# Kernel tuning notes

Hardware: AMD Instinct MI355X
Metric: run time of the kernel (lower is better)

The kernel has to match this reference:

```python
import jax, jax.numpy as jnp
import numpy as np

B, N, C, H, D = 1, 256, 128, 4, 32  # batch, seq, c_z, no_heads, c_hidden
INF = 1e9
LN_EPS = 1e-5


def setup_inputs() -> dict:
    key = jax.random.key(0)
    ks = jax.random.split(key, 8)
    s = 0.02
    return {
        "x": jax.random.normal(ks[0], (B, N, N, C), jnp.float32),
        "mask": jnp.ones((B, N, N), jnp.float32),
        "ln_w": jnp.ones((C,), jnp.float32),
        "ln_b": jnp.zeros((C,), jnp.float32),
        "w_bias": jax.random.normal(ks[1], (H, C), jnp.float32) * s,  # tri-bias linear (no bias)
        "wq": jax.random.normal(ks[2], (C, H, D), jnp.float32) * s,
        "wk": jax.random.normal(ks[3], (C, H, D), jnp.float32) * s,
        "wv": jax.random.normal(ks[4], (C, H, D), jnp.float32) * s,
        "wg": jax.random.normal(ks[5], (C, H, D), jnp.float32) * s,
        "bg": jnp.ones((H * D,), jnp.float32),  # gating bias init = 1 (OpenFold)
        "wo": jax.random.normal(ks[6], (C, H * D), jnp.float32) * s,
        "bo": jnp.zeros((C,), jnp.float32),
    }


def reference(x, mask, ln_w, ln_b, w_bias, wq, wk, wv, wg, bg, wo, bo):
    scale = 1.0 / np.sqrt(D)
    # Ending-node: transpose the two N dims, then operate like starting node
    x_t = jnp.swapaxes(x, 1, 2)          # [B, J, I, C] -> treat as [B, N, N, C]
    m_t = jnp.swapaxes(mask, 1, 2)       # [B, N, N]
    # layer norm over channels
    mu = jnp.mean(x_t, axis=-1, keepdims=True)
    var = jnp.var(x_t, axis=-1, keepdims=True)
    xn = (x_t - mu) * jax.lax.rsqrt(var + LN_EPS) * ln_w + ln_b
    # mask bias: inf * (mask - 1), broadcast over heads and query dim
    mask_bias = INF * (m_t[:, :, None, None, :] - 1.0)     # [B, N, 1, 1, N]
    # triangle bias: linear -> permute_final_dims (2,0,1) -> unsqueeze(-4)
    tri_bias = jnp.einsum("bijc,hc->bhij", xn, w_bias)[:, None]  # [B, 1, H, N, N]
    # gated MHA over the last sequence axis
    q = jnp.einsum("bijc,chd->bijhd", xn, wq) * scale
    k = jnp.einsum("bijc,chd->bijhd", xn, wk)
    v = jnp.einsum("bijc,chd->bijhd", xn, wv)
    a = jnp.einsum("bijhd,bikhd->bihjk", q, k) + mask_bias + tri_bias  # [B,N,H,N,N]
    a = jax.nn.softmax(a, axis=-1)
    o = jnp.einsum("bihjk,bikhd->bijhd", a, v)                        # [B,N,N,H,D]
    g = jax.nn.sigmoid(jnp.einsum("bijc,chd->bijhd", xn, wg) + bg.reshape(H, D))
    o = (o * g).reshape(B, N, N, H * D)
    out = jnp.einsum("bijk,ok->bijo", o, wo) + bo                     # [B,N,N,C]
    return jnp.swapaxes(out, 1, 2)
```

## Files before the change

kernel.cpp:

```cpp
#include <hip/hip_runtime.h>

#define N 256
#define C 128
#define H 4
#define D 32
#define LN_EPS 1e-5f
#define INFB 1e9f
#define SCALE 0.17677669529663687f

typedef __bf16 bf16x8 __attribute__((ext_vector_type(8)));
typedef __bf16 bf16x4 __attribute__((ext_vector_type(4)));
typedef __bf16 bf16x2 __attribute__((ext_vector_type(2)));
typedef _Float16 halfx8 __attribute__((ext_vector_type(8)));
typedef float floatx4 __attribute__((ext_vector_type(4)));

__device__ __forceinline__ floatx4 mfma16(bf16x8 a, bf16x8 b, floatx4 c) {
    return __builtin_amdgcn_mfma_f32_16x16x32_bf16(a, b, c, 0, 0, 0);
}
__device__ __forceinline__ floatx4 mfma16h(halfx8 a, halfx8 b, floatx4 c) {
    return __builtin_amdgcn_mfma_f32_16x16x32_f16(a, b, c, 0, 0, 0);
}

__global__ __launch_bounds__(256) void wt_kernel(
    const float* __restrict__ wq, const float* __restrict__ wk,
    const float* __restrict__ wv, const float* __restrict__ wg,
    const float* __restrict__ wo, __bf16* __restrict__ wTg,
    _Float16* __restrict__ woh)
{
    const int mat = blockIdx.x >> 3, seg = blockIdx.x & 7;
    if (mat == 4) {
        #pragma unroll
        for (int rep = 0; rep < 8; ++rep) {
            const int idx = seg * 2048 + rep * 256 + threadIdx.x;
            woh[idx] = (_Float16)wo[idx];
        }
        return;
    }
    const float* __restrict__ ws_ = (mat == 0) ? wq : (mat == 1) ? wk
                                  : (mat == 2) ? wv : wg;
    #pragma unroll
    for (int rep = 0; rep < 8; ++rep) {
        const int idx = seg * 2048 + rep * 256 + threadIdx.x;
        const int n = idx >> 7, c = idx & 127;
        wTg[mat * 16384 + n * 128 + c] = (__bf16)ws_[c * 128 + n];
    }
}

__global__ __launch_bounds__(256) void ln_kernel(
    const float* __restrict__ x, const float* __restrict__ lnw,
    const float* __restrict__ lnb, const float* __restrict__ wbias,
    __bf16* __restrict__ xn, float* __restrict__ tbp)
{
    const int t = threadIdx.x;
    const int wv = t >> 6, half = (t >> 5) & 1, lane = t & 31;
    const int r = blockIdx.x * 8 + wv * 2 + half;
    const int a = r >> 8, b = r & 255;

    const float4 v = *(const float4*)&x[((size_t)b * N + a) * C + lane * 4];
    float s  = v.x + v.y + v.z + v.w;
    float ss = v.x*v.x + v.y*v.y + v.z*v.z + v.w*v.w;
    #pragma unroll
    for (int o = 16; o; o >>= 1) {
        s  += __shfl_xor(s,  o);
        ss += __shfl_xor(ss, o);
    }
    const float mu  = s * (1.0f / 128.0f);
    const float var = ss * (1.0f / 128.0f) - mu * mu;
    const float rs  = rsqrtf(var + LN_EPS);

    const float4 lw = *(const float4*)&lnw[lane * 4];
    const float4 lb = *(const float4*)&lnb[lane * 4];
    const float y0 = (v.x - mu) * rs * lw.x + lb.x;
    const float y1 = (v.y - mu) * rs * lw.y + lb.y;
    const float y2 = (v.z - mu) * rs * lw.z + lb.z;
    const float y3 = (v.w - mu) * rs * lw.w + lb.w;

    bf16x4 xo;
    xo[0] = (__bf16)y0; xo[1] = (__bf16)y1;
    xo[2] = (__bf16)y2; xo[3] = (__bf16)y3;
    *(bf16x4*)&xn[(size_t)r * C + lane * 4] = xo;

    const int jb   = a >> 4;
    const int lnA  = (b & 15) | (((a & 15) >> 2) << 4);
    const int slot = ((b >> 4) << 2) | (a & 3);
    #pragma unroll
    for (int hh = 0; hh < H; ++hh) {
        const float4 wb4 = *(const float4*)&wbias[hh * C + lane * 4];
        float tv = y0 * wb4.x + y1 * wb4.y + y2 * wb4.z + y3 * wb4.w;
        #pragma unroll
        for (int o = 16; o; o >>= 1) tv += __shfl_xor(tv, o);
        if (lane == 0)
            tbp[(size_t)(((hh * 16 + jb) * 64 + lnA) * 64 + slot)] = tv;
    }
}

__global__ __launch_bounds__(256, 3) void proj_kernel(
    const __bf16* __restrict__ xn, const __bf16* __restrict__ wTg,
    __bf16* __restrict__ qbuf, __bf16* __restrict__ kbuf,
    __bf16* __restrict__ vbuf, __bf16* __restrict__ gbuf)
{
    __shared__ __bf16 Cs[4][64 * 72];

    const int t = threadIdx.x, w = t >> 6, lane = t & 63;
    const int ln16 = lane & 15, quad = lane >> 4;
    const int wr = w >> 1, wc = w & 1;
    const int m_base = blockIdx.x * 128 + wr * 64;
    const int n_base = wc * 64;
    const floatx4 z4 = {0.f, 0.f, 0.f, 0.f};

    const int m = m_base + lane;
    const int i = m >> 8, jk = m & 255;
    __bf16* __restrict__ Cw = &Cs[w][0];

    #pragma unroll 1
    for (int mat = 0; mat < 4; ++mat) {
        const __bf16* __restrict__ wT = wTg + mat * 16384;

        floatx4 Cf[4][4];
        #pragma unroll
        for (int mt = 0; mt < 4; ++mt)
            #pragma unroll
            for (int nt = 0; nt < 4; ++nt) Cf[mt][nt] = z4;

        #pragma unroll
        for (int ks = 0; ks < 4; ++ks) {
            bf16x8 Af[4], Bf[4];
            #pragma unroll
            for (int mt = 0; mt < 4; ++mt)
                Af[mt] = *(const bf16x8*)&xn[(size_t)(m_base + mt*16 + ln16) * 128 + ks*32 + quad*8];
            #pragma unroll
            for (int nt = 0; nt < 4; ++nt)
                Bf[nt] = *(const bf16x8*)&wT[(n_base + nt*16 + ln16) * 128 + ks*32 + quad*8];
            #pragma unroll
            for (int mt = 0; mt < 4; ++mt)
                #pragma unroll
                for (int nt = 0; nt < 4; ++nt)
                    Cf[mt][nt] = mfma16(Af[mt], Bf[nt], Cf[mt][nt]);
        }

        const float scl = (mat == 0) ? SCALE : 1.0f;
        #pragma unroll
        for (int mt = 0; mt < 4; ++mt)
            #pragma unroll
            for (int nt = 0; nt < 4; ++nt)
                #pragma unroll
                for (int r = 0; r < 4; ++r)
                    Cw[(mt*16 + quad*4 + r) * 72 + nt*16 + ln16] =
                        (__bf16)(Cf[mt][nt][r] * scl);

        __bf16* __restrict__ dst = (mat == 0) ? qbuf : (mat == 1) ? kbuf
                                 : (mat == 2) ? vbuf : gbuf;
        #pragma unroll
        for (int hf = 0; hf < 2; ++hf) {
            const int hh = wc * 2 + hf;
            __bf16* __restrict__ drow = dst + (((size_t)i*4 + hh)*256 + jk)*32;
            #pragma unroll
            for (int u = 0; u < 4; ++u)
                *(bf16x8*)&drow[u*8] = *(const bf16x8*)&Cw[lane*72 + hf*32 + u*8];
        }
    }
}

__global__ __launch_bounds__(256, 2) void attn_kernel(
    const float* __restrict__ tbp, const float* __restrict__ mask,
    const float* __restrict__ bg,
    const __bf16* __restrict__ qbuf, const __bf16* __restrict__ kbuf,
    const __bf16* __restrict__ vbuf, const __bf16* __restrict__ gbuf,
    _Float16* __restrict__ ogh)
{
    const int bid = blockIdx.x;
    const int i = bid & 255, h = bid >> 8;
    const int t = threadIdx.x, w = t >> 6, lane = t & 63;
    const int ln16 = lane & 15, quad = lane >> 4;

    __shared__ __align__(16) __bf16 Ks[256 * 32];
    __shared__ __align__(16) __bf16 VT[32 * 264];
    __shared__ __align__(16) __bf16 Pw[4][16 * 40];
    __shared__ float mb[256];

    const size_t hb = (size_t)i * 4 + h;
    const __bf16* __restrict__ qb = qbuf + hb * 8192;
    const __bf16* __restrict__ kb = kbuf + hb * 8192;
    const __bf16* __restrict__ vb = vbuf + hb * 8192;
    const __bf16* __restrict__ gb = gbuf + hb * 8192;

    {
        const int xt = (t & 3) ^ ((t >> 2) & 3);
        #pragma unroll
        for (int u = 0; u < 4; ++u)
            *(bf16x8*)&Ks[t * 32 + ((u ^ xt) * 8)] = *(const bf16x8*)&kb[t * 32 + u * 8];
    }
    #pragma unroll
    for (int u = 0; u < 4; ++u) {
        const bf16x8 vv = *(const bf16x8*)&vb[t * 32 + u * 8];
        #pragma unroll
        for (int e = 0; e < 8; ++e) VT[(u*8 + e) * 264 + t] = vv[e];
    }
    mb[t] = INFB * (mask[(size_t)t * N + i] - 1.0f);
    __syncthreads();

    const float bg0 = bg[h*32 + ln16], bg1 = bg[h*32 + 16 + ln16];

    float mbv[16];
    #pragma unroll
    for (int kt = 0; kt < 16; ++kt) mbv[kt] = mb[kt*16 + ln16];

    const int kq = ((quad ^ ((ln16 & 3) ^ ((ln16 >> 2) & 3))) * 8);

    __bf16* __restrict__ Pww = &Pw[w][0];
    const floatx4 z4 = {0.f, 0.f, 0.f, 0.f};
    _Float16* __restrict__ ogb = ogh + ((size_t)h * 256 + i) * 8192;

    #pragma unroll 1
    for (int jt = 0; jt < 4; ++jt) {
        const int jrow0 = w*64 + jt*16;
        const float* __restrict__ tbl =
            tbp + ((size_t)((h*16 + (w*4 + jt))*64 + lane) << 6);
        const bf16x8 Qf = *(const bf16x8*)&qb[(jrow0 + ln16)*32 + quad*8];

        floatx4 S[16];
        #pragma unroll
        for (int kt = 0; kt < 16; ++kt) {
            const float4 tb4 = *(const float4*)&tbl[kt*4];
            const float mbk = mbv[kt];
            floatx4 c;
            c[0] = mbk + tb4.x;
            c[1] = mbk + tb4.y;
            c[2] = mbk + tb4.z;
            c[3] = mbk + tb4.w;
            const bf16x8 Kf = *(const bf16x8*)&Ks[(kt*16 + ln16)*32 + kq];
            S[kt] = mfma16(Qf, Kf, c);
        }

        float mrow[4], l[4];
        #pragma unroll
        for (int r = 0; r < 4; ++r) {
            float mx = S[0][r];
            #pragma unroll
            for (int kt = 1; kt < 16; ++kt) mx = fmaxf(mx, S[kt][r]);
            #pragma unroll
            for (int off = 1; off < 16; off <<= 1) mx = fmaxf(mx, __shfl_xor(mx, off));
            mrow[r] = mx; l[r] = 0.f;
        }
        #pragma unroll
        for (int kt = 0; kt < 16; ++kt)
            #pragma unroll
            for (int r = 0; r < 4; ++r) {
                const float p = __expf(S[kt][r] - mrow[r]);
                S[kt][r] = p; l[r] += p;
            }
        #pragma unroll
        for (int r = 0; r < 4; ++r)
            #pragma unroll
            for (int off = 1; off < 16; off <<= 1) l[r] += __shfl_xor(l[r], off);

        floatx4 O0 = z4, O1 = z4;
        #pragma unroll
        for (int ch = 0; ch < 8; ++ch) {
            #pragma unroll
            for (int kk = 0; kk < 2; ++kk) {
                const int kt = ch*2 + kk;
                #pragma unroll
                for (int r = 0; r < 4; ++r)
                    Pww[(quad*4 + r)*40 + kk*16 + ln16] = (__bf16)S[kt][r];
            }
            const bf16x8 Af = *(const bf16x8*)&Pww[ln16*40 + quad*8];
            const bf16x8 V0 = *(const bf16x8*)&VT[ln16*264 + ch*32 + quad*8];
            const bf16x8 V1 = *(const bf16x8*)&VT[(16 + ln16)*264 + ch*32 + quad*8];
            O0 = mfma16(Af, V0, O0);
            O1 = mfma16(Af, V1, O1);
        }

        _Float16* Po = (_Float16*)Pww;
        #pragma unroll
        for (int r = 0; r < 4; ++r) {
            const float inv = 1.0f / l[r];
            const int jrow = jrow0 + quad*4 + r;
            const float g0 = (float)gb[jrow*32 + ln16];
            const float g1 = (float)gb[jrow*32 + 16 + ln16];
            const float gate0 = 1.0f / (1.0f + __expf(-(g0 + bg0)));
            const float gate1 = 1.0f / (1.0f + __expf(-(g1 + bg1)));
            Po[(quad*4 + r)*40 + ln16]      = (_Float16)(O0[r] * inv * gate0);
            Po[(quad*4 + r)*40 + 16 + ln16] = (_Float16)(O1[r] * inv * gate1);
        }
        {
            const int rr = lane >> 2, cc = lane & 3;
            const halfx8 ov = *(const halfx8*)&Po[rr*40 + cc*8];
            *(halfx8*)&ogb[(size_t)(jrow0 + rr)*32 + cc*8] = ov;
        }
    }
}

__global__ __launch_bounds__(256, 4) void outproj_kernel(
    const _Float16* __restrict__ og, const _Float16* __restrict__ woh,
    const float* __restrict__ bo, float* __restrict__ out)
{
    const int t = threadIdx.x, w = t >> 6, lane = t & 63;
    const int ln16 = lane & 15, quad = lane >> 4;
    const int wr = w >> 1, wc = w & 1;
    const int m_base = blockIdx.x * 128 + wr * 64;
    const int n_base = wc * 64;

    floatx4 Cf[4][4];
    const floatx4 z4 = {0.f, 0.f, 0.f, 0.f};
    #pragma unroll
    for (int mt = 0; mt < 4; ++mt)
        #pragma unroll
        for (int nt = 0; nt < 4; ++nt) Cf[mt][nt] = z4;

    #pragma unroll
    for (int ks = 0; ks < 4; ++ks) {
        halfx8 Af[4], Bf[4];
        #pragma unroll
        for (int mt = 0; mt < 4; ++mt)
            Af[mt] = *(const halfx8*)&og[(size_t)ks*2097152 + (size_t)(m_base + mt*16 + ln16)*32 + quad*8];
        #pragma unroll
        for (int nt = 0; nt < 4; ++nt)
            Bf[nt] = *(const halfx8*)&woh[(n_base + nt*16 + ln16)*128 + ks*32 + quad*8];
        #pragma unroll
        for (int mt = 0; mt < 4; ++mt)
            #pragma unroll
            for (int nt = 0; nt < 4; ++nt)
                Cf[mt][nt] = mfma16h(Af[mt], Bf[nt], Cf[mt][nt]);
    }

    float bov[4];
    #pragma unroll
    for (int nt = 0; nt < 4; ++nt) bov[nt] = bo[n_base + nt*16 + ln16];

    #pragma unroll
    for (int mt = 0; mt < 4; ++mt)
        #pragma unroll
        for (int r = 0; r < 4; ++r) {
            const int m = m_base + mt*16 + quad*4 + r;
            const size_t orow = (size_t)(m & 255) * 256 + (m >> 8);
            #pragma unroll
            for (int nt = 0; nt < 4; ++nt)
                out[orow*128 + n_base + nt*16 + ln16] = Cf[mt][nt][r] + bov[nt];
        }
}

extern "C" void kernel_launch(void* const* d_in, const int* in_sizes, int n_in,
                              void* d_out, int out_size, void* d_ws, size_t ws_size,
                              hipStream_t stream) {
    const float* x     = (const float*)d_in[0];
    const float* mask  = (const float*)d_in[1];
    const float* lnw   = (const float*)d_in[2];
    const float* lnb   = (const float*)d_in[3];
    const float* wbias = (const float*)d_in[4];
    const float* wq    = (const float*)d_in[5];
    const float* wk    = (const float*)d_in[6];
    const float* wv    = (const float*)d_in[7];
    const float* wg    = (const float*)d_in[8];
    const float* bg    = (const float*)d_in[9];
    const float* wo    = (const float*)d_in[10];
    const float* bo    = (const float*)d_in[11];
    float* out = (float*)d_out;

    char* wsb = (char*)d_ws;
    __bf16*    xn   = (__bf16*)   (wsb);
    float*     tbp  = (float*)    (wsb + 16777216);
    __bf16*    wTg  = (__bf16*)   (wsb + 17825792);
    _Float16*  woh  = (_Float16*) (wsb + 17956864);
    __bf16*    qbuf = (__bf16*)   (wsb + 17989632);
    __bf16*    kbuf = (__bf16*)   (wsb + 34766848);
    __bf16*    vbuf = (__bf16*)   (wsb + 51544064);
    __bf16*    gbuf = (__bf16*)   (wsb + 68321280);
    _Float16*  ogh  = (_Float16*) (wsb + 85098496);

    wt_kernel<<<40, 256, 0, stream>>>(wq, wk, wv, wg, wo, wTg, woh);
    ln_kernel<<<8192, 256, 0, stream>>>(x, lnw, lnb, wbias, xn, tbp);
    proj_kernel<<<512, 256, 0, stream>>>(xn, wTg, qbuf, kbuf, vbuf, gbuf);
    attn_kernel<<<1024, 256, 0, stream>>>(tbp, mask, bg, qbuf, kbuf, vbuf, gbuf, ogh);
    outproj_kernel<<<512, 256, 0, stream>>>(ogh, woh, bo, out);
}
```

Measured before the change: 239.2 us.

## Fuse layernorm into projection kernel, staging normalized rows in shared memory

The separate layernorm kernel is merged into the QKVG projection kernel. Each block normalizes its own 128 rows straight into LDS, also writing the triangle bias, then runs the MFMA projections reading A from LDS. This removes the global round trip of the bf16 normalized activations and one launch. In exchange, LDS use per block rises and the layernorm phase runs serially before the matmuls with lower occupancy (launch bounds 2).

Result: faster. 220.6 us (-7.8%).

```diff
diff --git a/kernel.cpp b/kernel.cpp
--- a/kernel.cpp
+++ b/kernel.cpp
@@ -46,69 +46,75 @@
     }
 }
 
-__global__ __launch_bounds__(256) void ln_kernel(
+__global__ __launch_bounds__(256, 2) void lnproj_kernel(
     const float* __restrict__ x, const float* __restrict__ lnw,
     const float* __restrict__ lnb, const float* __restrict__ wbias,
-    __bf16* __restrict__ xn, float* __restrict__ tbp)
-{
-    const int t = threadIdx.x;
-    const int wv = t >> 6, half = (t >> 5) & 1, lane = t & 31;
-    const int r = blockIdx.x * 8 + wv * 2 + half;
-    const int a = r >> 8, b = r & 255;
-
-    const float4 v = *(const float4*)&x[((size_t)b * N + a) * C + lane * 4];
-    float s  = v.x + v.y + v.z + v.w;
-    float ss = v.x*v.x + v.y*v.y + v.z*v.z + v.w*v.w;
-    #pragma unroll
-    for (int o = 16; o; o >>= 1) {
-        s  += __shfl_xor(s,  o);
-        ss += __shfl_xor(ss, o);
-    }
-    const float mu  = s * (1.0f / 128.0f);
-    const float var = ss * (1.0f / 128.0f) - mu * mu;
-    const float rs  = rsqrtf(var + LN_EPS);
-
-    const float4 lw = *(const float4*)&lnw[lane * 4];
-    const float4 lb = *(const float4*)&lnb[lane * 4];
-    const float y0 = (v.x - mu) * rs * lw.x + lb.x;
-    const float y1 = (v.y - mu) * rs * lw.y + lb.y;
-    const float y2 = (v.z - mu) * rs * lw.z + lb.z;
-    const float y3 = (v.w - mu) * rs * lw.w + lb.w;
-
-    bf16x4 xo;
-    xo[0] = (__bf16)y0; xo[1] = (__bf16)y1;
-    xo[2] = (__bf16)y2; xo[3] = (__bf16)y3;
-    *(bf16x4*)&xn[(size_t)r * C + lane * 4] = xo;
-
-    const int jb   = a >> 4;
-    const int lnA  = (b & 15) | (((a & 15) >> 2) << 4);
-    const int slot = ((b >> 4) << 2) | (a & 3);
-    #pragma unroll
-    for (int hh = 0; hh < H; ++hh) {
-        const float4 wb4 = *(const float4*)&wbias[hh * C + lane * 4];
-        float tv = y0 * wb4.x + y1 * wb4.y + y2 * wb4.z + y3 * wb4.w;
-        #pragma unroll
-        for (int o = 16; o; o >>= 1) tv += __shfl_xor(tv, o);
-        if (lane == 0)
-            tbp[(size_t)(((hh * 16 + jb) * 64 + lnA) * 64 + slot)] = tv;
-    }
-}
-
-__global__ __launch_bounds__(256, 3) void proj_kernel(
-    const __bf16* __restrict__ xn, const __bf16* __restrict__ wTg,
+    const __bf16* __restrict__ wTg, float* __restrict__ tbp,
     __bf16* __restrict__ qbuf, __bf16* __restrict__ kbuf,
     __bf16* __restrict__ vbuf, __bf16* __restrict__ gbuf)
 {
-    __shared__ __bf16 Cs[4][64 * 72];
-
-    const int t = threadIdx.x, w = t >> 6, lane = t & 63;
+    __shared__ __align__(16) __bf16 Als[128 * 136];
+    __shared__ __align__(16) __bf16 Cs[4][64 * 72];
+
+    const int t = threadIdx.x;
+    const int blk = blockIdx.x;
+
+    {
+        const int wv = t >> 6, half = (t >> 5) & 1, lane = t & 31;
+        #pragma unroll 1
+        for (int p = 0; p < 16; ++p) {
+            const int rl = p * 8 + wv * 2 + half;
+            const int r = blk * 128 + rl;
+            const int a = r >> 8, b = r & 255;
+
+            const float4 v = *(const float4*)&x[((size_t)b * N + a) * C + lane * 4];
+            float s  = v.x + v.y + v.z + v.w;
+            float ss = v.x*v.x + v.y*v.y + v.z*v.z + v.w*v.w;
+            #pragma unroll
+            for (int o = 16; o; o >>= 1) {
+                s  += __shfl_xor(s,  o);
+                ss += __shfl_xor(ss, o);
+            }
+            const float mu  = s * (1.0f / 128.0f);
+            const float var = ss * (1.0f / 128.0f) - mu * mu;
+            const float rs  = rsqrtf(var + LN_EPS);
+
+            const float4 lw = *(const float4*)&lnw[lane * 4];
+            const float4 lb = *(const float4*)&lnb[lane * 4];
+            const float y0 = (v.x - mu) * rs * lw.x + lb.x;
+            const float y1 = (v.y - mu) * rs * lw.y + lb.y;
+            const float y2 = (v.z - mu) * rs * lw.z + lb.z;
+            const float y3 = (v.w - mu) * rs * lw.w + lb.w;
+
+            bf16x4 xo;
+            xo[0] = (__bf16)y0; xo[1] = (__bf16)y1;
+            xo[2] = (__bf16)y2; xo[3] = (__bf16)y3;
+            *(bf16x4*)&Als[rl * 136 + lane * 4] = xo;
+
+            const int jb   = a >> 4;
+            const int lnA  = (b & 15) | (((a & 15) >> 2) << 4);
+            const int slot = ((b >> 4) << 2) | (a & 3);
+            #pragma unroll
+            for (int hh = 0; hh < H; ++hh) {
+                const float4 wb4 = *(const float4*)&wbias[hh * C + lane * 4];
+                float tv = y0 * wb4.x + y1 * wb4.y + y2 * wb4.z + y3 * wb4.w;
+                #pragma unroll
+                for (int o = 16; o; o >>= 1) tv += __shfl_xor(tv, o);
+                if (lane == 0)
+                    tbp[(size_t)(((hh * 16 + jb) * 64 + lnA) * 64 + slot)] = tv;
+            }
+        }
+    }
+    __syncthreads();
+
+    const int w = t >> 6, lane = t & 63;
     const int ln16 = lane & 15, quad = lane >> 4;
     const int wr = w >> 1, wc = w & 1;
-    const int m_base = blockIdx.x * 128 + wr * 64;
+    const int m_base_l = wr * 64;
     const int n_base = wc * 64;
     const floatx4 z4 = {0.f, 0.f, 0.f, 0.f};
 
-    const int m = m_base + lane;
+    const int m = blk * 128 + m_base_l + lane;
     const int i = m >> 8, jk = m & 255;
     __bf16* __restrict__ Cw = &Cs[w][0];
 
@@ -127,7 +133,7 @@
             bf16x8 Af[4], Bf[4];
             #pragma unroll
             for (int mt = 0; mt < 4; ++mt)
-                Af[mt] = *(const bf16x8*)&xn[(size_t)(m_base + mt*16 + ln16) * 128 + ks*32 + quad*8];
+                Af[mt] = *(const bf16x8*)&Als[(m_base_l + mt*16 + ln16) * 136 + ks*32 + quad*8];
             #pragma unroll
             for (int nt = 0; nt < 4; ++nt)
                 Bf[nt] = *(const bf16x8*)&wT[(n_base + nt*16 + ln16) * 128 + ks*32 + quad*8];
@@ -358,7 +364,6 @@
     float* out = (float*)d_out;
 
     char* wsb = (char*)d_ws;
-    __bf16*    xn   = (__bf16*)   (wsb);
     float*     tbp  = (float*)    (wsb + 16777216);
     __bf16*    wTg  = (__bf16*)   (wsb + 17825792);
     _Float16*  woh  = (_Float16*) (wsb + 17956864);
@@ -369,8 +374,8 @@
     _Float16*  ogh  = (_Float16*) (wsb + 85098496);
 
     wt_kernel<<<40, 256, 0, stream>>>(wq, wk, wv, wg, wo, wTg, woh);
-    ln_kernel<<<8192, 256, 0, stream>>>(x, lnw, lnb, wbias, xn, tbp);
-    proj_kernel<<<512, 256, 0, stream>>>(xn, wTg, qbuf, kbuf, vbuf, gbuf);
+    lnproj_kernel<<<512, 256, 0, stream>>>(x, lnw, lnb, wbias, wTg, tbp,
+                                           qbuf, kbuf, vbuf, gbuf);
     attn_kernel<<<1024, 256, 0, stream>>>(tbp, mask, bg, qbuf, kbuf, vbuf, gbuf, ogh);
     outproj_kernel<<<512, 256, 0, stream>>>(ogh, woh, bo, out);
 }
```
